# Optimization experiments

Hardware: AMD Instinct MI355X
Metric: run time of the kernel (lower is better)

The kernel has to match this reference:

```python
import jax, jax.numpy as jnp
import numpy as np

D_MODEL = 768
NUM_HEADS = 12
HEAD_DIM = D_MODEL // NUM_HEADS
B, S = 2, 2048


def setup_inputs() -> dict:
    key = jax.random.key(0)
    ks = jax.random.split(key, 12)
    s = 1.0 / np.sqrt(D_MODEL)
    inp = {
        "query": jax.random.normal(ks[0], (B, S, D_MODEL), jnp.float32),
        "key": jax.random.normal(ks[1], (B, S, D_MODEL), jnp.float32),
        "value": jax.random.normal(ks[2], (B, S, D_MODEL), jnp.float32),
        # causal mask; masked_fill(scores, mask == 0, -inf)
        "mask": jnp.tril(jnp.ones((S, S), jnp.int32))[None, None, :, :],
        "Wq": jax.random.uniform(ks[3], (D_MODEL, D_MODEL), jnp.float32, -s, s),
        "bq": jax.random.uniform(ks[4], (D_MODEL,), jnp.float32, -s, s),
        "Wk": jax.random.uniform(ks[5], (D_MODEL, D_MODEL), jnp.float32, -s, s),
        "bk": jax.random.uniform(ks[6], (D_MODEL,), jnp.float32, -s, s),
        "Wv": jax.random.uniform(ks[7], (D_MODEL, D_MODEL), jnp.float32, -s, s),
        "bv": jax.random.uniform(ks[8], (D_MODEL,), jnp.float32, -s, s),
        "Wo": jax.random.uniform(ks[9], (D_MODEL, D_MODEL), jnp.float32, -s, s),
        "bo": jax.random.uniform(ks[10], (D_MODEL,), jnp.float32, -s, s),
    }
    return inp


def reference(query, key, value, mask, Wq, bq, Wk, bk, Wv, bv, Wo, bo):
    Bq, Lq, Dm = query.shape
    Lk = key.shape[1]
    H, Dh = NUM_HEADS, HEAD_DIM
    # projections (torch Linear: x @ W.T + b), split into heads -> [B,H,L,Dh]
    q = (query @ Wq.T + bq).reshape(Bq, Lq, H, Dh).transpose(0, 2, 1, 3)
    k = (key @ Wk.T + bk).reshape(Bq, Lk, H, Dh).transpose(0, 2, 1, 3)
    v = (value @ Wv.T + bv).reshape(Bq, Lk, H, Dh).transpose(0, 2, 1, 3)
    scores = jnp.einsum("bhqd,bhkd->bhqk", q, k) / jnp.sqrt(jnp.float32(Dh))
    scores = jnp.where(mask == 0, -jnp.inf, scores)
    attn = jax.nn.softmax(scores, axis=-1)
    context = jnp.einsum("bhqk,bhkd->bhqd", attn, v)
    context = context.transpose(0, 2, 1, 3).reshape(Bq, Lq, Dm)
    return context @ Wo.T + bo
```

## Files before the change

### kernel.cpp

```cpp
#include <hip/hip_runtime.h>

#define DM    768
#define NH    12
#define NB    2
#define DHD   64
#define SQL   2048
#define MROWS 4096
#define WSZ   589824
#define XSZ   3145728
#define QSCALE 0.18033688f

typedef short  s16x8 __attribute__((ext_vector_type(8)));
typedef float  f32x4 __attribute__((ext_vector_type(4)));
typedef float  f32x16 __attribute__((ext_vector_type(16)));
typedef unsigned short u16x4 __attribute__((ext_vector_type(4)));
typedef unsigned short u16x8 __attribute__((ext_vector_type(8)));
typedef unsigned int   u32x4 __attribute__((ext_vector_type(4)));

static __device__ __forceinline__ unsigned short f2bf(float f) {
    unsigned int u = __builtin_bit_cast(unsigned int, f);
    u += 0x7FFFu + ((u >> 16) & 1u);
    return (unsigned short)(u >> 16);
}

static __device__ __forceinline__ unsigned int cvtpk1(float x, float y) {
    unsigned int r;
    asm("v_cvt_pk_bf16_f32 %0, %1, %2" : "=v"(r) : "v"(x), "v"(y));
    return r;
}

static __device__ __forceinline__ uint2 cvt2(float4 v) {
    return (uint2){cvtpk1(v.x, v.y), cvtpk1(v.z, v.w)};
}

static __device__ __forceinline__ f32x4 mfma16(s16x8 a, s16x8 b, f32x4 c) {
    return __builtin_amdgcn_mfma_f32_16x16x32_bf16(a, b, c, 0, 0, 0);
}
static __device__ __forceinline__ f32x16 mfma32(s16x8 a, s16x8 b, f32x16 c) {
    return __builtin_amdgcn_mfma_f32_32x32x16_bf16(a, b, c, 0, 0, 0);
}

__global__ __launch_bounds__(256)
void prepW(const float* __restrict__ Wq, const float* __restrict__ Wk,
           const float* __restrict__ Wv, const float* __restrict__ Wo,
           unsigned short* __restrict__ Wb)
{
    const int z = blockIdx.y;
    const float* src = (z == 0) ? Wq : (z == 1) ? Wk : (z == 2) ? Wv : Wo;
    unsigned short* d = Wb + (size_t)z * WSZ;
    const int i = blockIdx.x * 256 + threadIdx.x;
    float4 a = *reinterpret_cast<const float4*>(&src[(size_t)i * 8]);
    float4 b = *reinterpret_cast<const float4*>(&src[(size_t)i * 8 + 4]);
    uint2 p0 = cvt2(a), p1 = cvt2(b);
    u32x4 pk = {p0.x, p0.y, p1.x, p1.y};
    *reinterpret_cast<u32x4*>(&d[(size_t)i * 8]) = pk;
}

__global__ __launch_bounds__(512)
void qkv_proj(const float* __restrict__ Xq, const float* __restrict__ Xk,
              const float* __restrict__ Xv,
              const unsigned short* __restrict__ Wb,
              const float* __restrict__ bq, const float* __restrict__ bk,
              const float* __restrict__ bv,
              unsigned short* __restrict__ Qo, unsigned short* __restrict__ Ko,
              unsigned short* __restrict__ Vo)
{
    const int z = blockIdx.z;
    const float* X = (z == 0) ? Xq : (z == 1) ? Xk : Xv;
    const unsigned short* W = Wb + (size_t)z * WSZ;
    const float* bias = (z == 0) ? bq : (z == 1) ? bk : bv;
    unsigned short* O = (z == 0) ? Qo : (z == 1) ? Ko : Vo;

    __shared__ unsigned short As[2][128][72];
    __shared__ unsigned short Bs[2][128][72];

    const int tid  = threadIdx.x;
    const int lane = tid & 63;
    const int w    = tid >> 6;
    const int wm   = w >> 1, wn = w & 1;
    const int l15  = lane & 15, lg = lane >> 4;
    const int m0   = blockIdx.y * 128;
    const int n0   = blockIdx.x * 128;
    const int ar   = tid >> 2, ac = (tid & 3) << 4;

    f32x4 acc[2][4];
    #pragma unroll
    for (int i = 0; i < 2; ++i)
        #pragma unroll
        for (int j = 0; j < 4; ++j)
            acc[i][j] = (f32x4){0.f, 0.f, 0.f, 0.f};

    float4 ra[4]; u16x8 rb[2];
    #pragma unroll
    for (int i = 0; i < 4; ++i)
        ra[i] = *reinterpret_cast<const float4*>(&X[(size_t)(m0 + ar) * DM + ac + i * 4]);
    #pragma unroll
    for (int i = 0; i < 2; ++i)
        rb[i] = *reinterpret_cast<const u16x8*>(&W[(size_t)(n0 + ar) * DM + ac + i * 8]);
    #pragma unroll
    for (int i = 0; i < 4; ++i)
        *reinterpret_cast<uint2*>(&As[0][ar][ac + i * 4]) = cvt2(ra[i]);
    #pragma unroll
    for (int i = 0; i < 2; ++i)
        *reinterpret_cast<u16x8*>(&Bs[0][ar][ac + i * 8]) = rb[i];
    __syncthreads();

    int c = 0;
    for (int k0 = 0; k0 < DM; k0 += 64) {
        const bool more = (k0 + 64 < DM);
        if (more) {
            #pragma unroll
            for (int i = 0; i < 4; ++i)
                ra[i] = *reinterpret_cast<const float4*>(&X[(size_t)(m0 + ar) * DM + k0 + 64 + ac + i * 4]);
            #pragma unroll
            for (int i = 0; i < 2; ++i)
                rb[i] = *reinterpret_cast<const u16x8*>(&W[(size_t)(n0 + ar) * DM + k0 + 64 + ac + i * 8]);
        }
        s16x8 af[2][2], bfg[4][2];
        #pragma unroll
        for (int mi = 0; mi < 2; ++mi)
            #pragma unroll
            for (int ks = 0; ks < 2; ++ks)
                af[mi][ks] = *reinterpret_cast<const s16x8*>(&As[c][wm * 32 + mi * 16 + l15][ks * 32 + lg * 8]);
        #pragma unroll
        for (int nj = 0; nj < 4; ++nj)
            #pragma unroll
            for (int ks = 0; ks < 2; ++ks)
                bfg[nj][ks] = *reinterpret_cast<const s16x8*>(&Bs[c][wn * 64 + nj * 16 + l15][ks * 32 + lg * 8]);
        #pragma unroll
        for (int mi = 0; mi < 2; ++mi)
            #pragma unroll
            for (int nj = 0; nj < 4; ++nj)
                #pragma unroll
                for (int ks = 0; ks < 2; ++ks)
                    acc[mi][nj] = mfma16(af[mi][ks], bfg[nj][ks], acc[mi][nj]);
        if (more) {
            #pragma unroll
            for (int i = 0; i < 4; ++i)
                *reinterpret_cast<uint2*>(&As[c ^ 1][ar][ac + i * 4]) = cvt2(ra[i]);
            #pragma unroll
            for (int i = 0; i < 2; ++i)
                *reinterpret_cast<u16x8*>(&Bs[c ^ 1][ar][ac + i * 8]) = rb[i];
        }
        __syncthreads();
        c ^= 1;
    }

    const float scale = (z == 0) ? QSCALE : 1.0f;
    #pragma unroll
    for (int mi = 0; mi < 2; ++mi) {
        #pragma unroll
        for (int nj = 0; nj < 4; ++nj) {
            int col = n0 + wn * 64 + nj * 16 + l15;
            float bb = bias[col];
            int hh = col >> 6, d = col & 63;
            if (z < 2) {
                #pragma unroll
                for (int r = 0; r < 4; ++r) {
                    int row = m0 + wm * 32 + mi * 16 + (lg << 2) + r;
                    int b = row >> 11, s = row & (SQL - 1);
                    O[(((size_t)(b * NH + hh) * SQL) + s) * DHD + d] =
                        f2bf((acc[mi][nj][r] + bb) * scale);
                }
            } else {
                int row = m0 + wm * 32 + mi * 16 + (lg << 2);
                int b = row >> 11, s = row & (SQL - 1);
                u16x4 pk;
                #pragma unroll
                for (int r = 0; r < 4; ++r) pk[r] = f2bf(acc[mi][nj][r] + bb);
                *reinterpret_cast<u16x4*>(&O[(((size_t)(b * NH + hh) * DHD) + d) * SQL + s]) = pk;
            }
        }
    }
}

__global__ __launch_bounds__(512)
void attn(const unsigned short* __restrict__ Q, const unsigned short* __restrict__ K,
          const unsigned short* __restrict__ Vt, unsigned short* __restrict__ Ctx)
{
    __shared__ float Acc[8][2112];

    const int tid  = threadIdx.x;
    const int lane = tid & 63;
    const int w    = tid >> 6;
    const int hi   = lane >> 5;
    const int l31  = lane & 31;

    const int id  = blockIdx.x;
    const int xcd = id & 7;
    const int rr  = id >> 3;
    const int bh  = xcd * 3 + (rr % 3);
    const int qt  = 63 - rr / 3;
    const int q0  = qt * 32;

    const unsigned short* Qb = Q  + (size_t)bh * SQL * DHD;
    const unsigned short* Kb = K  + (size_t)bh * SQL * DHD;
    const unsigned short* Vb = Vt + (size_t)bh * DHD * SQL;

    s16x8 qf[4];
    #pragma unroll
    for (int t = 0; t < 4; ++t)
        qf[t] = *reinterpret_cast<const s16x8*>(&Qb[(size_t)(q0 + l31) * DHD + t * 16 + hi * 8]);

    f32x16 o0 = {}, o1 = {};
    float m = -__builtin_inff(), l = 0.f;
    const int nkt = (q0 >> 5) + 1;

    int cnt = (w < nkt) ? ((nkt - w + 7) >> 3) : 0;
    int kt  = w;

    s16x8 kA[4], kB[4];
    if (cnt >= 2) {
        const int ka = kt * 32, kb2 = (kt + 8) * 32;
        #pragma unroll
        for (int t = 0; t < 4; ++t) {
            kA[t] = *reinterpret_cast<const s16x8*>(&Kb[(size_t)(ka + l31) * DHD + t * 16 + hi * 8]);
            kB[t] = *reinterpret_cast<const s16x8*>(&Kb[(size_t)(kb2 + l31) * DHD + t * 16 + hi * 8]);
        }
    } else if (cnt == 1) {
        const int ka = kt * 32;
        #pragma unroll
        for (int t = 0; t < 4; ++t)
            kA[t] = *reinterpret_cast<const s16x8*>(&Kb[(size_t)(ka + l31) * DHD + t * 16 + hi * 8]);
    }

    while (cnt >= 2) {
        const int ka = kt * 32, kb2 = (kt + 8) * 32;

        s16x8 va00 = *reinterpret_cast<const s16x8*>(&Vb[(size_t)(l31)      * SQL + ka + hi * 8]);
        s16x8 va01 = *reinterpret_cast<const s16x8*>(&Vb[(size_t)(l31)      * SQL + ka + 16 + hi * 8]);
        s16x8 va10 = *reinterpret_cast<const s16x8*>(&Vb[(size_t)(32 + l31) * SQL + ka + hi * 8]);
        s16x8 va11 = *reinterpret_cast<const s16x8*>(&Vb[(size_t)(32 + l31) * SQL + ka + 16 + hi * 8]);
        s16x8 vb00 = *reinterpret_cast<const s16x8*>(&Vb[(size_t)(l31)      * SQL + kb2 + hi * 8]);
        s16x8 vb01 = *reinterpret_cast<const s16x8*>(&Vb[(size_t)(l31)      * SQL + kb2 + 16 + hi * 8]);
        s16x8 vb10 = *reinterpret_cast<const s16x8*>(&Vb[(size_t)(32 + l31) * SQL + kb2 + hi * 8]);
        s16x8 vb11 = *reinterpret_cast<const s16x8*>(&Vb[(size_t)(32 + l31) * SQL + kb2 + 16 + hi * 8]);

        f32x16 sa = {}, sb = {};
        #pragma unroll
        for (int t = 0; t < 4; ++t) sa = mfma32(kA[t], qf[t], sa);
        #pragma unroll
        for (int t = 0; t < 4; ++t) sb = mfma32(kB[t], qf[t], sb);

        const int ncnt = cnt - 2, nkt2 = kt + 16;
        if (ncnt >= 2) {
            const int na = nkt2 * 32, nb = (nkt2 + 8) * 32;
            #pragma unroll
            for (int t = 0; t < 4; ++t) {
                kA[t] = *reinterpret_cast<const s16x8*>(&Kb[(size_t)(na + l31) * DHD + t * 16 + hi * 8]);
                kB[t] = *reinterpret_cast<const s16x8*>(&Kb[(size_t)(nb + l31) * DHD + t * 16 + hi * 8]);
            }
        } else if (ncnt == 1) {
            const int na = nkt2 * 32;
            #pragma unroll
            for (int t = 0; t < 4; ++t)
                kA[t] = *reinterpret_cast<const s16x8*>(&Kb[(size_t)(na + l31) * DHD + t * 16 + hi * 8]);
        }

        if (kt + 8 == nkt - 1) {
            #pragma unroll
            for (int r = 0; r < 16; ++r) {
                int kvr = (r & 3) + 8 * (r >> 2) + 4 * hi;
                if (kvr > l31) sb[r] = -1.0e30f;
            }
        }

        float pm = fmaxf(sa[0], sb[0]);
        #pragma unroll
        for (int r = 1; r < 16; ++r) pm = fmaxf(pm, fmaxf(sa[r], sb[r]));
        pm = fmaxf(pm, __shfl_xor(pm, 32));

        if (!__all(pm <= m)) {
            const float mn = fmaxf(m, pm);
            const float al = __builtin_amdgcn_exp2f(m - mn);
            m = mn;
            l *= al;
            #pragma unroll
            for (int r = 0; r < 16; ++r) { o0[r] *= al; o1[r] *= al; }
        }

        float rs = 0.f;
        #pragma unroll
        for (int r = 0; r < 16; ++r) {
            sa[r] = __builtin_amdgcn_exp2f(sa[r] - m); rs += sa[r];
            sb[r] = __builtin_amdgcn_exp2f(sb[r] - m); rs += sb[r];
        }
        rs += __shfl_xor(rs, 32);
        l += rs;

        s16x8 pfa[2], pfb[2];
        #pragma unroll
        for (int ks = 0; ks < 2; ++ks) {
            const int rb = ks * 8;
            unsigned int a0 = cvtpk1(sa[rb + 0], sa[rb + 1]);
            unsigned int b0 = cvtpk1(sa[rb + 4], sa[rb + 5]);
            asm("v_permlane32_swap_b32 %0, %1" : "+v"(a0), "+v"(b0));
            unsigned int a1 = cvtpk1(sa[rb + 2], sa[rb + 3]);
            unsigned int b1 = cvtpk1(sa[rb + 6], sa[rb + 7]);
            asm("v_permlane32_swap_b32 %0, %1" : "+v"(a1), "+v"(b1));
            u32x4 pw = {a0, a1, b0, b1};
            pfa[ks] = __builtin_bit_cast(s16x8, pw);
        }
        #pragma unroll
        for (int ks = 0; ks < 2; ++ks) {
            const int rb = ks * 8;
            unsigned int a0 = cvtpk1(sb[rb + 0], sb[rb + 1]);
            unsigned int b0 = cvtpk1(sb[rb + 4], sb[rb + 5]);
            asm("v_permlane32_swap_b32 %0, %1" : "+v"(a0), "+v"(b0));
            unsigned int a1 = cvtpk1(sb[rb + 2], sb[rb + 3]);
            unsigned int b1 = cvtpk1(sb[rb + 6], sb[rb + 7]);
            asm("v_permlane32_swap_b32 %0, %1" : "+v"(a1), "+v"(b1));
            u32x4 pw = {a0, a1, b0, b1};
            pfb[ks] = __builtin_bit_cast(s16x8, pw);
        }

        o0 = mfma32(va00, pfa[0], o0);
        o0 = mfma32(va01, pfa[1], o0);
        o1 = mfma32(va10, pfa[0], o1);
        o1 = mfma32(va11, pfa[1], o1);
        o0 = mfma32(vb00, pfb[0], o0);
        o0 = mfma32(vb01, pfb[1], o0);
        o1 = mfma32(vb10, pfb[0], o1);
        o1 = mfma32(vb11, pfb[1], o1);

        kt = nkt2; cnt = ncnt;
    }

    if (cnt) {
        const int ka = kt * 32;
        s16x8 va00 = *reinterpret_cast<const s16x8*>(&Vb[(size_t)(l31)      * SQL + ka + hi * 8]);
        s16x8 va01 = *reinterpret_cast<const s16x8*>(&Vb[(size_t)(l31)      * SQL + ka + 16 + hi * 8]);
        s16x8 va10 = *reinterpret_cast<const s16x8*>(&Vb[(size_t)(32 + l31) * SQL + ka + hi * 8]);
        s16x8 va11 = *reinterpret_cast<const s16x8*>(&Vb[(size_t)(32 + l31) * SQL + ka + 16 + hi * 8]);

        f32x16 sa = {};
        #pragma unroll
        for (int t = 0; t < 4; ++t) sa = mfma32(kA[t], qf[t], sa);

        if (kt == nkt - 1) {
            #pragma unroll
            for (int r = 0; r < 16; ++r) {
                int kvr = (r & 3) + 8 * (r >> 2) + 4 * hi;
                if (kvr > l31) sa[r] = -1.0e30f;
            }
        }

        float pm = sa[0];
        #pragma unroll
        for (int r = 1; r < 16; ++r) pm = fmaxf(pm, sa[r]);
        pm = fmaxf(pm, __shfl_xor(pm, 32));

        if (!__all(pm <= m)) {
            const float mn = fmaxf(m, pm);
            const float al = __builtin_amdgcn_exp2f(m - mn);
            m = mn;
            l *= al;
            #pragma unroll
            for (int r = 0; r < 16; ++r) { o0[r] *= al; o1[r] *= al; }
        }

        float rs = 0.f;
        #pragma unroll
        for (int r = 0; r < 16; ++r) {
            sa[r] = __builtin_amdgcn_exp2f(sa[r] - m); rs += sa[r];
        }
        rs += __shfl_xor(rs, 32);
        l += rs;

        s16x8 pfa[2];
        #pragma unroll
        for (int ks = 0; ks < 2; ++ks) {
            const int rb = ks * 8;
            unsigned int a0 = cvtpk1(sa[rb + 0], sa[rb + 1]);
            unsigned int b0 = cvtpk1(sa[rb + 4], sa[rb + 5]);
            asm("v_permlane32_swap_b32 %0, %1" : "+v"(a0), "+v"(b0));
            unsigned int a1 = cvtpk1(sa[rb + 2], sa[rb + 3]);
            unsigned int b1 = cvtpk1(sa[rb + 6], sa[rb + 7]);
            asm("v_permlane32_swap_b32 %0, %1" : "+v"(a1), "+v"(b1));
            u32x4 pw = {a0, a1, b0, b1};
            pfa[ks] = __builtin_bit_cast(s16x8, pw);
        }

        o0 = mfma32(va00, pfa[0], o0);
        o0 = mfma32(va01, pfa[1], o0);
        o1 = mfma32(va10, pfa[0], o1);
        o1 = mfma32(va11, pfa[1], o1);
    }

    #pragma unroll
    for (int r = 0; r < 16; ++r) {
        int d = (r & 3) + 8 * (r >> 2) + 4 * hi;
        Acc[w][d * 32 + l31]        = o0[r];
        Acc[w][(32 + d) * 32 + l31] = o1[r];
    }
    if (hi == 0) { Acc[w][2048 + l31] = m; Acc[w][2080 + l31] = l; }
    __syncthreads();

    {
        const int q  = tid & 31;
        const int d4 = (tid >> 5) << 2;
        float M = -__builtin_inff();
        float mv[8];
        #pragma unroll
        for (int j = 0; j < 8; ++j) { mv[j] = Acc[j][2048 + q]; M = fmaxf(M, mv[j]); }
        float f[8]; float L = 0.f;
        #pragma unroll
        for (int j = 0; j < 8; ++j) {
            f[j] = __builtin_amdgcn_exp2f(mv[j] - M);
            L += f[j] * Acc[j][2080 + q];
        }
        const float invL = 1.0f / L;
        const int b = bh / NH, h = bh % NH;
        u16x4 pk;
        #pragma unroll
        for (int jj = 0; jj < 4; ++jj) {
            int d = d4 + jj;
            float o = 0.f;
            #pragma unroll
            for (int j = 0; j < 8; ++j) o += f[j] * Acc[j][d * 32 + q];
            pk[jj] = f2bf(o * invL);
        }
        *reinterpret_cast<u16x4*>(&Ctx[(((size_t)(b * SQL + q0 + q) * NH) + h) * DHD + d4]) = pk;
    }
}

__global__ __launch_bounds__(256)
void out_proj(const unsigned short* __restrict__ Ctx, const unsigned short* __restrict__ Wob,
              const float* __restrict__ bo, float* __restrict__ Out)
{
    __shared__ unsigned short As[2][64][72];
    __shared__ unsigned short Bs[2][64][72];

    const int tid  = threadIdx.x;
    const int lane = tid & 63;
    const int w    = tid >> 6;
    const int wm   = w >> 1, wn = w & 1;
    const int l15  = lane & 15, lg = lane >> 4;
    const int m0   = blockIdx.y * 64;
    const int n0   = blockIdx.x * 64;
    const int ar   = tid >> 2, ac = (tid & 3) << 4;

    f32x4 acc[2][2];
    #pragma unroll
    for (int i = 0; i < 2; ++i)
        #pragma unroll
        for (int j = 0; j < 2; ++j)
            acc[i][j] = (f32x4){0.f, 0.f, 0.f, 0.f};

    u16x8 ra[2], rb[2];
    #pragma unroll
    for (int i = 0; i < 2; ++i) {
        ra[i] = *reinterpret_cast<const u16x8*>(&Ctx[(size_t)(m0 + ar) * DM + ac + i * 8]);
        rb[i] = *reinterpret_cast<const u16x8*>(&Wob[(size_t)(n0 + ar) * DM + ac + i * 8]);
    }
    #pragma unroll
    for (int i = 0; i < 2; ++i) {
        *reinterpret_cast<u16x8*>(&As[0][ar][ac + i * 8]) = ra[i];
        *reinterpret_cast<u16x8*>(&Bs[0][ar][ac + i * 8]) = rb[i];
    }
    __syncthreads();

    int c = 0;
    for (int k0 = 0; k0 < DM; k0 += 64) {
        const bool more = (k0 + 64 < DM);
        if (more) {
            #pragma unroll
            for (int i = 0; i < 2; ++i) {
                ra[i] = *reinterpret_cast<const u16x8*>(&Ctx[(size_t)(m0 + ar) * DM + k0 + 64 + ac + i * 8]);
                rb[i] = *reinterpret_cast<const u16x8*>(&Wob[(size_t)(n0 + ar) * DM + k0 + 64 + ac + i * 8]);
            }
        }
        s16x8 af[2][2], bfg[2][2];
        #pragma unroll
        for (int mi = 0; mi < 2; ++mi)
            #pragma unroll
            for (int ks = 0; ks < 2; ++ks) {
                af[mi][ks]  = *reinterpret_cast<const s16x8*>(&As[c][wm * 32 + mi * 16 + l15][ks * 32 + lg * 8]);
                bfg[mi][ks] = *reinterpret_cast<const s16x8*>(&Bs[c][wn * 32 + mi * 16 + l15][ks * 32 + lg * 8]);
            }
        #pragma unroll
        for (int mi = 0; mi < 2; ++mi)
            #pragma unroll
            for (int nj = 0; nj < 2; ++nj)
                #pragma unroll
                for (int ks = 0; ks < 2; ++ks)
                    acc[mi][nj] = mfma16(af[mi][ks], bfg[nj][ks], acc[mi][nj]);
        if (more) {
            #pragma unroll
            for (int i = 0; i < 2; ++i) {
                *reinterpret_cast<u16x8*>(&As[c ^ 1][ar][ac + i * 8]) = ra[i];
                *reinterpret_cast<u16x8*>(&Bs[c ^ 1][ar][ac + i * 8]) = rb[i];
            }
        }
        __syncthreads();
        c ^= 1;
    }

    #pragma unroll
    for (int mi = 0; mi < 2; ++mi)
        #pragma unroll
        for (int nj = 0; nj < 2; ++nj) {
            int col = n0 + wn * 32 + nj * 16 + l15;
            float bb = bo[col];
            #pragma unroll
            for (int r = 0; r < 4; ++r) {
                int row = m0 + wm * 32 + mi * 16 + (lg << 2) + r;
                Out[(size_t)row * DM + col] = acc[mi][nj][r] + bb;
            }
        }
}

extern "C" void kernel_launch(void* const* d_in, const int* in_sizes, int n_in,
                              void* d_out, int out_size, void* d_ws, size_t ws_size,
                              hipStream_t stream) {
    const float* query = (const float*)d_in[0];
    const float* key   = (const float*)d_in[1];
    const float* value = (const float*)d_in[2];
    const float* Wq = (const float*)d_in[4];
    const float* bq = (const float*)d_in[5];
    const float* Wk = (const float*)d_in[6];
    const float* bk = (const float*)d_in[7];
    const float* Wv = (const float*)d_in[8];
    const float* bv = (const float*)d_in[9];
    const float* Wo = (const float*)d_in[10];
    const float* bo = (const float*)d_in[11];
    float* out = (float*)d_out;

    unsigned short* Wb  = (unsigned short*)d_ws;
    unsigned short* Qb  = Wb  + (size_t)4 * WSZ;
    unsigned short* Kb  = Qb  + (size_t)XSZ;
    unsigned short* Vtb = Kb  + (size_t)XSZ;
    unsigned short* Ctx = Vtb + (size_t)XSZ;

    prepW<<<dim3(288, 4), 256, 0, stream>>>(Wq, Wk, Wv, Wo, Wb);
    qkv_proj<<<dim3(6, 32, 3), 512, 0, stream>>>(query, key, value, Wb,
                                                 bq, bk, bv, Qb, Kb, Vtb);
    attn<<<dim3(NB * NH * 64), 512, 0, stream>>>(Qb, Kb, Vtb, Ctx);
    out_proj<<<dim3(12, 64), 256, 0, stream>>>(Ctx, Wb + (size_t)3 * WSZ, bo, out);
}
```

Baseline: 236.3 us.

## Remap GEMM blocks per XCD, shrink QKV tiles, single-buffer shared memory

Both projection GEMMs now use a flat 1D grid whose block IDs are decoded so that consecutive M tiles land on the same XCD, which should improve L2 reuse of the activation rows and weights. The QKV projection tile drops from 128x128 with 512 threads to 64x128 with 256 threads, giving more blocks for occupancy. Shared memory becomes single-buffered with an extra barrier per k-step, trading less LDS for more synchronisation stalls.

```diff
diff --git a/kernel.cpp b/kernel.cpp
--- a/kernel.cpp
+++ b/kernel.cpp
@@ -56,7 +56,7 @@
     *reinterpret_cast<u32x4*>(&d[(size_t)i * 8]) = pk;
 }
 
-__global__ __launch_bounds__(512)
+__global__ __launch_bounds__(256)
 void qkv_proj(const float* __restrict__ Xq, const float* __restrict__ Xk,
               const float* __restrict__ Xv,
               const unsigned short* __restrict__ Wb,
@@ -65,23 +65,31 @@
               unsigned short* __restrict__ Qo, unsigned short* __restrict__ Ko,
               unsigned short* __restrict__ Vo)
 {
-    const int z = blockIdx.z;
+    const int id  = blockIdx.x;
+    const int xcd = id & 7;
+    const int r0  = id >> 3;
+    const int z   = r0 / 48;
+    const int rem = r0 % 48;
+    const int ml  = rem / 6;
+    const int nb  = rem % 6;
+    const int m0  = (xcd * 8 + ml) * 64;
+    const int n0  = nb * 128;
+
     const float* X = (z == 0) ? Xq : (z == 1) ? Xk : Xv;
     const unsigned short* W = Wb + (size_t)z * WSZ;
     const float* bias = (z == 0) ? bq : (z == 1) ? bk : bv;
     unsigned short* O = (z == 0) ? Qo : (z == 1) ? Ko : Vo;
 
-    __shared__ unsigned short As[2][128][72];
-    __shared__ unsigned short Bs[2][128][72];
+    __shared__ unsigned short As[64][72];
+    __shared__ unsigned short Bs[128][72];
 
     const int tid  = threadIdx.x;
     const int lane = tid & 63;
     const int w    = tid >> 6;
     const int wm   = w >> 1, wn = w & 1;
     const int l15  = lane & 15, lg = lane >> 4;
-    const int m0   = blockIdx.y * 128;
-    const int n0   = blockIdx.x * 128;
     const int ar   = tid >> 2, ac = (tid & 3) << 4;
+    const int br   = tid >> 1, bc = (tid & 1) << 5;
 
     f32x4 acc[2][4];
     #pragma unroll
@@ -90,43 +98,39 @@
         for (int j = 0; j < 4; ++j)
             acc[i][j] = (f32x4){0.f, 0.f, 0.f, 0.f};
 
-    float4 ra[4]; u16x8 rb[2];
-    #pragma unroll
-    for (int i = 0; i < 4; ++i)
+    float4 ra[4]; u16x8 rb[4];
+    #pragma unroll
+    for (int i = 0; i < 4; ++i) {
         ra[i] = *reinterpret_cast<const float4*>(&X[(size_t)(m0 + ar) * DM + ac + i * 4]);
-    #pragma unroll
-    for (int i = 0; i < 2; ++i)
-        rb[i] = *reinterpret_cast<const u16x8*>(&W[(size_t)(n0 + ar) * DM + ac + i * 8]);
-    #pragma unroll
-    for (int i = 0; i < 4; ++i)
-        *reinterpret_cast<uint2*>(&As[0][ar][ac + i * 4]) = cvt2(ra[i]);
-    #pragma unroll
-    for (int i = 0; i < 2; ++i)
-        *reinterpret_cast<u16x8*>(&Bs[0][ar][ac + i * 8]) = rb[i];
+        rb[i] = *reinterpret_cast<const u16x8*>(&W[(size_t)(n0 + br) * DM + bc + i * 8]);
+    }
+    #pragma unroll
+    for (int i = 0; i < 4; ++i) {
+        *reinterpret_cast<uint2*>(&As[ar][ac + i * 4]) = cvt2(ra[i]);
+        *reinterpret_cast<u16x8*>(&Bs[br][bc + i * 8]) = rb[i];
+    }
     __syncthreads();
 
-    int c = 0;
     for (int k0 = 0; k0 < DM; k0 += 64) {
         const bool more = (k0 + 64 < DM);
         if (more) {
             #pragma unroll
-            for (int i = 0; i < 4; ++i)
+            for (int i = 0; i < 4; ++i) {
                 ra[i] = *reinterpret_cast<const float4*>(&X[(size_t)(m0 + ar) * DM + k0 + 64 + ac + i * 4]);
-            #pragma unroll
-            for (int i = 0; i < 2; ++i)
-                rb[i] = *reinterpret_cast<const u16x8*>(&W[(size_t)(n0 + ar) * DM + k0 + 64 + ac + i * 8]);
+                rb[i] = *reinterpret_cast<const u16x8*>(&W[(size_t)(n0 + br) * DM + k0 + 64 + bc + i * 8]);
+            }
         }
         s16x8 af[2][2], bfg[4][2];
         #pragma unroll
         for (int mi = 0; mi < 2; ++mi)
             #pragma unroll
             for (int ks = 0; ks < 2; ++ks)
-                af[mi][ks] = *reinterpret_cast<const s16x8*>(&As[c][wm * 32 + mi * 16 + l15][ks * 32 + lg * 8]);
+                af[mi][ks] = *reinterpret_cast<const s16x8*>(&As[wm * 32 + mi * 16 + l15][ks * 32 + lg * 8]);
         #pragma unroll
         for (int nj = 0; nj < 4; ++nj)
             #pragma unroll
             for (int ks = 0; ks < 2; ++ks)
-                bfg[nj][ks] = *reinterpret_cast<const s16x8*>(&Bs[c][wn * 64 + nj * 16 + l15][ks * 32 + lg * 8]);
+                bfg[nj][ks] = *reinterpret_cast<const s16x8*>(&Bs[wn * 64 + nj * 16 + l15][ks * 32 + lg * 8]);
         #pragma unroll
         for (int mi = 0; mi < 2; ++mi)
             #pragma unroll
@@ -134,16 +138,15 @@
                 #pragma unroll
                 for (int ks = 0; ks < 2; ++ks)
                     acc[mi][nj] = mfma16(af[mi][ks], bfg[nj][ks], acc[mi][nj]);
+        __syncthreads();
         if (more) {
             #pragma unroll
-            for (int i = 0; i < 4; ++i)
-                *reinterpret_cast<uint2*>(&As[c ^ 1][ar][ac + i * 4]) = cvt2(ra[i]);
-            #pragma unroll
-            for (int i = 0; i < 2; ++i)
-                *reinterpret_cast<u16x8*>(&Bs[c ^ 1][ar][ac + i * 8]) = rb[i];
-        }
-        __syncthreads();
-        c ^= 1;
+            for (int i = 0; i < 4; ++i) {
+                *reinterpret_cast<uint2*>(&As[ar][ac + i * 4]) = cvt2(ra[i]);
+                *reinterpret_cast<u16x8*>(&Bs[br][bc + i * 8]) = rb[i];
+            }
+            __syncthreads();
+        }
     }
 
     const float scale = (z == 0) ? QSCALE : 1.0f;
@@ -428,16 +431,22 @@
 void out_proj(const unsigned short* __restrict__ Ctx, const unsigned short* __restrict__ Wob,
               const float* __restrict__ bo, float* __restrict__ Out)
 {
-    __shared__ unsigned short As[2][64][72];
-    __shared__ unsigned short Bs[2][64][72];
+    __shared__ unsigned short As[64][72];
+    __shared__ unsigned short Bs[64][72];
+
+    const int id  = blockIdx.x;
+    const int xcd = id & 7;
+    const int r2  = id >> 3;
+    const int ml  = r2 / 12;
+    const int nb  = r2 % 12;
+    const int m0  = (xcd * 8 + ml) * 64;
+    const int n0  = nb * 64;
 
     const int tid  = threadIdx.x;
     const int lane = tid & 63;
     const int w    = tid >> 6;
     const int wm   = w >> 1, wn = w & 1;
     const int l15  = lane & 15, lg = lane >> 4;
-    const int m0   = blockIdx.y * 64;
-    const int n0   = blockIdx.x * 64;
     const int ar   = tid >> 2, ac = (tid & 3) << 4;
 
     f32x4 acc[2][2];
@@ -455,12 +464,11 @@
     }
     #pragma unroll
     for (int i = 0; i < 2; ++i) {
-        *reinterpret_cast<u16x8*>(&As[0][ar][ac + i * 8]) = ra[i];
-        *reinterpret_cast<u16x8*>(&Bs[0][ar][ac + i * 8]) = rb[i];
+        *reinterpret_cast<u16x8*>(&As[ar][ac + i * 8]) = ra[i];
+        *reinterpret_cast<u16x8*>(&Bs[ar][ac + i * 8]) = rb[i];
     }
     __syncthreads();
 
-    int c = 0;
     for (int k0 = 0; k0 < DM; k0 += 64) {
         const bool more = (k0 + 64 < DM);
         if (more) {
@@ -475,8 +483,8 @@
         for (int mi = 0; mi < 2; ++mi)
             #pragma unroll
             for (int ks = 0; ks < 2; ++ks) {
-                af[mi][ks]  = *reinterpret_cast<const s16x8*>(&As[c][wm * 32 + mi * 16 + l15][ks * 32 + lg * 8]);
-                bfg[mi][ks] = *reinterpret_cast<const s16x8*>(&Bs[c][wn * 32 + mi * 16 + l15][ks * 32 + lg * 8]);
+                af[mi][ks]  = *reinterpret_cast<const s16x8*>(&As[wm * 32 + mi * 16 + l15][ks * 32 + lg * 8]);
+                bfg[mi][ks] = *reinterpret_cast<const s16x8*>(&Bs[wn * 32 + mi * 16 + l15][ks * 32 + lg * 8]);
             }
         #pragma unroll
         for (int mi = 0; mi < 2; ++mi)
@@ -485,15 +493,15 @@
                 #pragma unroll
                 for (int ks = 0; ks < 2; ++ks)
                     acc[mi][nj] = mfma16(af[mi][ks], bfg[nj][ks], acc[mi][nj]);
+        __syncthreads();
         if (more) {
             #pragma unroll
             for (int i = 0; i < 2; ++i) {
-                *reinterpret_cast<u16x8*>(&As[c ^ 1][ar][ac + i * 8]) = ra[i];
-                *reinterpret_cast<u16x8*>(&Bs[c ^ 1][ar][ac + i * 8]) = rb[i];
-            }
-        }
-        __syncthreads();
-        c ^= 1;
+                *reinterpret_cast<u16x8*>(&As[ar][ac + i * 8]) = ra[i];
+                *reinterpret_cast<u16x8*>(&Bs[ar][ac + i * 8]) = rb[i];
+            }
+            __syncthreads();
+        }
     }
 
     #pragma unroll
@@ -533,8 +541,8 @@
     unsigned short* Ctx = Vtb + (size_t)XSZ;
 
     prepW<<<dim3(288, 4), 256, 0, stream>>>(Wq, Wk, Wv, Wo, Wb);
-    qkv_proj<<<dim3(6, 32, 3), 512, 0, stream>>>(query, key, value, Wb,
-                                                 bq, bk, bv, Qb, Kb, Vtb);
+    qkv_proj<<<dim3(1152), 256, 0, stream>>>(query, key, value, Wb,
+                                             bq, bk, bv, Qb, Kb, Vtb);
     attn<<<dim3(NB * NH * 64), 512, 0, stream>>>(Qb, Kb, Vtb, Ctx);
-    out_proj<<<dim3(12, 64), 256, 0, stream>>>(Ctx, Wb + (size_t)3 * WSZ, bo, out);
-}
+    out_proj<<<dim3(768), 256, 0, stream>>>(Ctx, Wb + (size_t)3 * WSZ, bo, out);
+}
```

After: 221.9 us. 1.07x faster.
